# Performance work log

Hardware: AMD Instinct MI355X
Metric: run time of the kernel (lower is better)

The kernel has to match this reference:

```python
import jax, jax.numpy as jnp
import numpy as np

B, N0, D0, N1, D1 = 128, 64, 32, 64, 32
K = 65  # depthwise conv kernel size
SCALE = 5.0
FOCUS = 3.0
EPS_Z = float(jnp.finfo(jnp.float32).eps)


def setup_inputs() -> dict:
    key = jax.random.key(0)
    k1, k2, k3, kw, kc, kb = jax.random.split(key, 6)
    x1 = jax.random.normal(k1, (B, N0, D0), dtype=jnp.float32)
    x2 = jax.random.normal(k2, (B, N0, D0), dtype=jnp.float32)
    x3 = jax.random.normal(k3, (B, N0, D0), dtype=jnp.float32)
    # kaiming_normal_ on W [N1, N0, D0, D1]: fan_in = N0*D0*D1 per torch default on 4D
    fan_in = N0 * D0 * D1
    W = jax.random.normal(kw, (N1, N0, D0, D1), dtype=jnp.float32) * np.sqrt(2.0 / fan_in)
    # Conv1d(N1*D1, N1*D1, K, groups=N1): weight [out_ch, in_ch/groups, K]
    cin_g = D1
    bound = 1.0 / np.sqrt(cin_g * K)
    conv_w = jax.random.uniform(kc, (N1 * D1, cin_g, K), dtype=jnp.float32, minval=-bound, maxval=bound)
    conv_b = jax.random.uniform(kb, (N1 * D1,), dtype=jnp.float32, minval=-bound, maxval=bound)
    return {"x1": x1, "x2": x2, "x3": x3, "W": W, "conv_w": conv_w, "conv_b": conv_b}


def _transform(x, W):
    # x: [B, N0, D0], W: [N1, N0, D0, D1] -> u: [B, N1*D1, N0]
    u = jnp.einsum('bji,kjiz->bkjz', x, W)        # [B, N1, N0, D1]
    u = jnp.transpose(u, (0, 1, 3, 2))             # [B, N1, D1, N0]
    return u.reshape(u.shape[0], N1 * D1, N0)


def _focus(u):
    # ReLU kernel + focusing-factor renormalization along last dim
    u = jax.nn.relu(u) + 1e-6
    u = u / SCALE
    n = jnp.linalg.norm(u, axis=-1, keepdims=True)
    up = u ** FOCUS
    return up / jnp.linalg.norm(up, axis=-1, keepdims=True) * n


def _squash(x, eps=1e-20):
    norm = jnp.linalg.norm(x, axis=-1, keepdims=True)
    coef = 1.0 - 1.0 / (jnp.exp(norm) + eps)
    return coef * (x / (norm + eps))


def reference(x1, x2, x3, W, conv_w, conv_b):
    u1 = _focus(_transform(x1, W))  # [B, N1*D1, N0]
    u2 = _focus(_transform(x2, W))
    u3 = _focus(_transform(x3, W))
    z = 1.0 / (jnp.einsum('bic,bc->bi', u1, u1.sum(axis=1)) + EPS_Z)  # [B, N1*D1]
    kv = jnp.einsum('bjc,bjd->bcd', u2, u3)                           # [B, N0, N0]
    x = jnp.einsum('bic,bcd,bi->bid', u1, kv, z)                      # [B, N1*D1, N0]
    # grouped (depthwise-per-capsule) conv1d, 'same' padding
    y = jax.lax.conv_general_dilated(
        x, conv_w, window_strides=(1,), padding=[(K // 2, K // 2)],
        dimension_numbers=('NCH', 'OIH', 'NCH'), feature_group_count=N1)
    y = y + conv_b[None, :, None]
    out = (x + y).sum(axis=-1).reshape(-1, N1, D1)  # [B, N1, D1]
    return _squash(out)
```

## Files before the change

### kernel.cpp

```cpp
#include <hip/hip_runtime.h>
#include <cstddef>

#define NB 128
#define NT 64
#define ND 32
#define NG 64
#define NC 2048
#define KW 65
#define EPSZ 1.1920928955078125e-07f

#define OFF_URAW 0ull
#define SZ_URAW  (3ull * NB * NT * NC)
#define OFF_F    (OFF_URAW + SZ_URAW)
#define SZ_F     (3ull * NB * NC)
#define OFF_S1   (OFF_F + SZ_F)
#define SZ_S1    ((unsigned long long)NB * NT)
#define OFF_KV   (OFF_S1 + SZ_S1)
#define SZ_KV    ((unsigned long long)NB * NT * NT)

__global__ __launch_bounds__(256) void k_transform(
    const float* __restrict__ x1, const float* __restrict__ x2,
    const float* __restrict__ x3, const float* __restrict__ W,
    float* __restrict__ uraw) {
  int bid = blockIdx.x;
  int j   = bid & 63;
  int nt  = (bid >> 6) & 15;
  int inp = bid >> 10;
  const float* x = (inp == 0) ? x1 : ((inp == 1) ? x2 : x3);
  float* uout = uraw + (size_t)inp * ((size_t)NB * NT * NC);

  __shared__ float as[32][132];
  __shared__ float bs[32][132];
  int tid = threadIdx.x;

  {
    int b = tid >> 1, h = tid & 1;
    const float* xp = x + ((size_t)b * NT + j) * ND + h * 16;
#pragma unroll
    for (int q = 0; q < 4; ++q) {
      float4 v = *reinterpret_cast<const float4*>(xp + q * 4);
      int i0 = h * 16 + q * 4;
      as[i0 + 0][b] = v.x; as[i0 + 1][b] = v.y;
      as[i0 + 2][b] = v.z; as[i0 + 3][b] = v.w;
    }
  }
  {
    int kk = tid >> 6, u = tid & 63;
    int i = u >> 1, h = u & 1;
    const float* wp = W + (((size_t)(nt * 4 + kk) * NT + j) * ND + i) * ND + h * 16;
#pragma unroll
    for (int q = 0; q < 4; ++q) {
      float4 v = *reinterpret_cast<const float4*>(wp + q * 4);
      int c0 = kk * 32 + h * 16 + q * 4;
      bs[i][c0 + 0] = v.x; bs[i][c0 + 1] = v.y;
      bs[i][c0 + 2] = v.z; bs[i][c0 + 3] = v.w;
    }
  }
  __syncthreads();

  int tm = tid & 15, tn = tid >> 4;
  int m0 = tm * 8, n0 = tn * 8;
  float acc[8][8];
#pragma unroll
  for (int a = 0; a < 8; ++a)
#pragma unroll
    for (int c = 0; c < 8; ++c) acc[a][c] = 0.f;

#pragma unroll 4
  for (int kk = 0; kk < 32; ++kk) {
    float4 a0 = *reinterpret_cast<const float4*>(&as[kk][m0]);
    float4 a1 = *reinterpret_cast<const float4*>(&as[kk][m0 + 4]);
    float4 b0 = *reinterpret_cast<const float4*>(&bs[kk][n0]);
    float4 b1 = *reinterpret_cast<const float4*>(&bs[kk][n0 + 4]);
    float av[8] = {a0.x, a0.y, a0.z, a0.w, a1.x, a1.y, a1.z, a1.w};
    float bv[8] = {b0.x, b0.y, b0.z, b0.w, b1.x, b1.y, b1.z, b1.w};
#pragma unroll
    for (int mi = 0; mi < 8; ++mi)
#pragma unroll
      for (int ni = 0; ni < 8; ++ni)
        acc[mi][ni] = fmaf(av[mi], bv[ni], acc[mi][ni]);
  }

#pragma unroll
  for (int mi = 0; mi < 8; ++mi) {
    float* cp = uout + ((size_t)(m0 + mi) * NT + j) * NC + nt * 128 + n0;
    float4 v0 = {acc[mi][0], acc[mi][1], acc[mi][2], acc[mi][3]};
    float4 v1 = {acc[mi][4], acc[mi][5], acc[mi][6], acc[mi][7]};
    *reinterpret_cast<float4*>(cp)     = v0;
    *reinterpret_cast<float4*>(cp + 4) = v1;
  }
}

__global__ __launch_bounds__(256) void k_factors(
    const float* __restrict__ uraw, float* __restrict__ f,
    float* __restrict__ s1) {
  int bid = blockIdx.x;
  int q = bid & 3, b = (bid >> 2) & 127, inp = bid >> 9;
  const float* u = uraw + ((size_t)inp * NB + b) * ((size_t)NT * NC);
  int tid = threadIdx.x;
  int ch = q * 512 + tid * 2;

  float s2a = 0.f, s6a = 0.f, s2b = 0.f, s6b = 0.f;
  for (int t = 0; t < NT; ++t) {
    float2 v = *reinterpret_cast<const float2*>(u + (size_t)t * NC + ch);
    float ua = (fmaxf(v.x, 0.f) + 1e-6f) * 0.2f;
    float p2a = ua * ua, p3a = p2a * ua;
    s2a += p2a; s6a += p3a * p3a;
    float ub = (fmaxf(v.y, 0.f) + 1e-6f) * 0.2f;
    float p2b = ub * ub, p3b = p2b * ub;
    s2b += p2b; s6b += p3b * p3b;
  }
  float fa = sqrtf(s2a) / sqrtf(s6a);
  float fb = sqrtf(s2b) / sqrtf(s6b);
  float2 fv = {fa, fb};
  *reinterpret_cast<float2*>(f + ((size_t)inp * NB + b) * NC + ch) = fv;

  if (inp == 0) {
    __shared__ float part[NT][4];
    int wid = tid >> 6, lane = tid & 63;
    for (int t = 0; t < NT; ++t) {
      float2 v = *reinterpret_cast<const float2*>(u + (size_t)t * NC + ch);
      float ua = (fmaxf(v.x, 0.f) + 1e-6f) * 0.2f;
      float ub = (fmaxf(v.y, 0.f) + 1e-6f) * 0.2f;
      float val = ua * ua * ua * fa + ub * ub * ub * fb;
#pragma unroll
      for (int m = 32; m >= 1; m >>= 1) val += __shfl_xor(val, m, 64);
      if (lane == 0) part[t][wid] = val;
    }
    __syncthreads();
    if (tid < NT)
      atomicAdd(&s1[b * NT + tid],
                part[tid][0] + part[tid][1] + part[tid][2] + part[tid][3]);
  }
}

__global__ void k_zero(float* __restrict__ p, int n) {
  int i = blockIdx.x * blockDim.x + threadIdx.x;
  int stride = gridDim.x * blockDim.x;
  for (; i < n; i += stride) p[i] = 0.f;
}

__global__ __launch_bounds__(256) void k_kv(
    const float* __restrict__ uraw, const float* __restrict__ f,
    float* __restrict__ kv) {
  int b = blockIdx.x >> 3, chq = blockIdx.x & 7;
  int chbase = chq * 256;
  const float* u2 = uraw + ((size_t)NB + b) * ((size_t)NT * NC);
  const float* u3 = uraw + (2ull * NB + b) * ((size_t)NT * NC);
  const float* f2 = f + ((size_t)NB + b) * NC;
  const float* f3 = f + (2ull * NB + b) * NC;

  __shared__ float a2[64][68];
  __shared__ float a3[64][68];
  int tid = threadIdx.x;

  int tm = tid & 15, tn = tid >> 4;
  float acc[4][4];
#pragma unroll
  for (int r = 0; r < 4; ++r)
#pragma unroll
    for (int q = 0; q < 4; ++q) acc[r][q] = 0.f;

  for (int tile = 0; tile < 4; ++tile) {
    int ch0 = chbase + tile * 64;
    __syncthreads();
    {
      int t = tid >> 2, c4 = tid & 3;
#pragma unroll
      for (int q = 0; q < 4; ++q) {
        int c = c4 * 16 + q * 4;
        float4 v2 = *reinterpret_cast<const float4*>(u2 + (size_t)t * NC + ch0 + c);
        float4 g2 = *reinterpret_cast<const float4*>(f2 + ch0 + c);
        float4 v3 = *reinterpret_cast<const float4*>(u3 + (size_t)t * NC + ch0 + c);
        float4 g3 = *reinterpret_cast<const float4*>(f3 + ch0 + c);
        float vv2[4] = {v2.x, v2.y, v2.z, v2.w};
        float gg2[4] = {g2.x, g2.y, g2.z, g2.w};
        float vv3[4] = {v3.x, v3.y, v3.z, v3.w};
        float gg3[4] = {g3.x, g3.y, g3.z, g3.w};
#pragma unroll
        for (int r = 0; r < 4; ++r) {
          float uu = (fmaxf(vv2[r], 0.f) + 1e-6f) * 0.2f;
          a2[c + r][t] = uu * uu * uu * gg2[r];
          float ww = (fmaxf(vv3[r], 0.f) + 1e-6f) * 0.2f;
          a3[c + r][t] = ww * ww * ww * gg3[r];
        }
      }
    }
    __syncthreads();
#pragma unroll 8
    for (int ch = 0; ch < 64; ++ch) {
      float4 av = *reinterpret_cast<const float4*>(&a2[ch][tm * 4]);
      float4 bv = *reinterpret_cast<const float4*>(&a3[ch][tn * 4]);
      float aa[4] = {av.x, av.y, av.z, av.w};
      float bb[4] = {bv.x, bv.y, bv.z, bv.w};
#pragma unroll
      for (int r = 0; r < 4; ++r)
#pragma unroll
        for (int q = 0; q < 4; ++q)
          acc[r][q] = fmaf(aa[r], bb[q], acc[r][q]);
    }
  }
#pragma unroll
  for (int r = 0; r < 4; ++r)
#pragma unroll
    for (int q = 0; q < 4; ++q)
      atomicAdd(&kv[(size_t)b * (NT * NT) + (tm * 4 + r) * NT + tn * 4 + q],
                acc[r][q]);
}

__global__ __launch_bounds__(64) void k_cwt(
    const float* __restrict__ cw, float* __restrict__ cwt) {
  int o = blockIdx.x;
  int tid = threadIdx.x;
  __shared__ float row[32 * KW];
  for (int i = tid; i < 32 * KW; i += 64) row[i] = cw[(size_t)o * (32 * KW) + i];
  __syncthreads();
  int jj = tid, j = jj + 1;
  for (int ci = 0; ci < 32; ++ci) {
    float v = 0.f;
    if (j <= 32) v -= row[ci * KW + j + 32];
    if (j >= 32 && j <= 63) v += row[ci * KW + j - 32];
    if (j == 64) {
      float s = 0.f;
      for (int k = 32; k <= 64; ++k) s += row[ci * KW + k];
      v += s;
    }
    cwt[(size_t)o * 2048 + ci * 64 + jj] = v;
  }
}

__global__ __launch_bounds__(256) void k_pre(
    const float* __restrict__ uraw, const float* __restrict__ f,
    const float* __restrict__ kvg, const float* __restrict__ s1g,
    float* __restrict__ pre) {
  int b = blockIdx.x >> 3, q = blockIdx.x & 7;
  int chbase = q * 256;
  const float* u1 = uraw + (size_t)b * ((size_t)NT * NC);
  const float* f1 = f + (size_t)b * NC;
  int tid = threadIdx.x;

  __shared__ float kvpreL[64][68];
  __shared__ float s1L[64];
  __shared__ float utL[64][132];

#pragma unroll
  for (int qq = 0; qq < 16; ++qq) {
    int i = tid + qq * 256;
    kvpreL[i >> 6][i & 63] = kvg[(size_t)b * (NT * NT) + i];
  }
  if (tid < 64) s1L[tid] = s1g[b * NT + tid];
  __syncthreads();
  if (tid < 64) {
    float run = 0.f;
    for (int t2 = 0; t2 < 64; ++t2) {
      run += kvpreL[tid][t2];
      kvpreL[tid][t2] = run;
    }
  }

  int cg = tid >> 3, tg = tid & 7;
  for (int tile = 0; tile < 2; ++tile) {
    int ch0 = chbase + tile * 128;
    __syncthreads();
    {
      int t = tid >> 2, c4 = tid & 3;
      const float* up = u1 + (size_t)t * NC + ch0 + c4 * 32;
      const float* fp = f1 + ch0 + c4 * 32;
#pragma unroll
      for (int qq = 0; qq < 8; ++qq) {
        float4 v  = *reinterpret_cast<const float4*>(up + qq * 4);
        float4 fv = *reinterpret_cast<const float4*>(fp + qq * 4);
        float vv[4] = {v.x, v.y, v.z, v.w};
        float ff[4] = {fv.x, fv.y, fv.z, fv.w};
#pragma unroll
        for (int r = 0; r < 4; ++r) {
          float uu = (fmaxf(vv[r], 0.f) + 1e-6f) * 0.2f;
          utL[t][c4 * 33 + qq * 4 + r] = uu * uu * uu * ff[r];
        }
      }
    }
    __syncthreads();

    int cl = cg * 4;
    int sk = (cl >> 5) * 33 + (cl & 31);
    float acc[4][8];
#pragma unroll
    for (int r = 0; r < 4; ++r)
#pragma unroll
      for (int c = 0; c < 8; ++c) acc[r][c] = 0.f;
    float accz[4] = {0.f, 0.f, 0.f, 0.f};

#pragma unroll 4
    for (int t1 = 0; t1 < 64; ++t1) {
      float4 a = *reinterpret_cast<const float4*>(&utL[t1][sk]);
      float s = s1L[t1];
      float4 k0 = *reinterpret_cast<const float4*>(&kvpreL[t1][tg * 8]);
      float4 k1 = *reinterpret_cast<const float4*>(&kvpreL[t1][tg * 8 + 4]);
      float aa[4] = {a.x, a.y, a.z, a.w};
      float kk[8] = {k0.x, k0.y, k0.z, k0.w, k1.x, k1.y, k1.z, k1.w};
#pragma unroll
      for (int r = 0; r < 4; ++r) {
        accz[r] = fmaf(aa[r], s, accz[r]);
#pragma unroll
        for (int c = 0; c < 8; ++c)
          acc[r][c] = fmaf(aa[r], kk[c], acc[r][c]);
      }
    }
#pragma unroll
    for (int r = 0; r < 4; ++r) {
      float z = 1.f / (accz[r] + EPSZ);
      float* pp = pre + ((size_t)b * NC + ch0 + cl + r) * 64 + tg * 8;
      float4 o0 = {acc[r][0] * z, acc[r][1] * z, acc[r][2] * z, acc[r][3] * z};
      float4 o1 = {acc[r][4] * z, acc[r][5] * z, acc[r][6] * z, acc[r][7] * z};
      *reinterpret_cast<float4*>(pp)     = o0;
      *reinterpret_cast<float4*>(pp + 4) = o1;
    }
  }
}

__global__ __launch_bounds__(256) void k_gemm(
    const float* __restrict__ pre, const float* __restrict__ cwt,
    float* __restrict__ ysum) {
  int g = blockIdx.x >> 3, ks = blockIdx.x & 7;
  int tid = threadIdx.x;
  int oh = tid & 7, bh = tid >> 3;

  __shared__ float AsT[64][132];
  __shared__ float BsT[64][36];

  float acc[4][4];
#pragma unroll
  for (int i = 0; i < 4; ++i)
#pragma unroll
    for (int j = 0; j < 4; ++j) acc[i][j] = 0.f;

  for (int kc = 0; kc < 4; ++kc) {
    int ci = ks * 4 + kc;
    __syncthreads();
    {
      int bb = tid >> 1, jh = (tid & 1) * 32;
      const float* ap = pre + ((size_t)bb * NC + g * 32 + ci) * 64 + jh;
#pragma unroll
      for (int qq = 0; qq < 8; ++qq) {
        float4 v = *reinterpret_cast<const float4*>(ap + qq * 4);
        int jj = jh + qq * 4;
        AsT[jj + 0][bb] = v.x; AsT[jj + 1][bb] = v.y;
        AsT[jj + 2][bb] = v.z; AsT[jj + 3][bb] = v.w;
      }
    }
    if (tid < 128) {
      int o = tid >> 2, jh = (tid & 3) * 16;
      const float* bp = cwt + (size_t)(g * 32 + o) * 2048 + ci * 64 + jh;
#pragma unroll
      for (int qq = 0; qq < 4; ++qq) {
        float4 v = *reinterpret_cast<const float4*>(bp + qq * 4);
        int jj = jh + qq * 4;
        BsT[jj + 0][o] = v.x; BsT[jj + 1][o] = v.y;
        BsT[jj + 2][o] = v.z; BsT[jj + 3][o] = v.w;
      }
    }
    __syncthreads();

#pragma unroll 8
    for (int jj = 0; jj < 64; ++jj) {
      float4 a = *reinterpret_cast<const float4*>(&AsT[jj][bh * 4]);
      float4 bv = *reinterpret_cast<const float4*>(&BsT[jj][oh * 4]);
      float aa[4] = {a.x, a.y, a.z, a.w};
      float bb[4] = {bv.x, bv.y, bv.z, bv.w};
#pragma unroll
      for (int i = 0; i < 4; ++i)
#pragma unroll
        for (int j = 0; j < 4; ++j)
          acc[i][j] = fmaf(aa[i], bb[j], acc[i][j]);
    }
  }

#pragma unroll
  for (int i = 0; i < 4; ++i)
#pragma unroll
    for (int j = 0; j < 4; ++j)
      atomicAdd(&ysum[(size_t)(bh * 4 + i) * NC + g * 32 + oh * 4 + j],
                acc[i][j]);
}

__global__ __launch_bounds__(256) void k_out(
    const float* __restrict__ pre, const float* __restrict__ ysum,
    const float* __restrict__ cb, float* __restrict__ out) {
  int tid = threadIdx.x;
  int b = blockIdx.x >> 3;
  int g = (blockIdx.x & 7) * 8 + (tid >> 5);
  int o = tid & 31;
  int go = g * 32 + o;
  float xs = pre[((size_t)b * NC + go) * 64 + 63];
  float val = ysum[(size_t)b * NC + go] + xs + 64.f * cb[go];
  float sq = val * val;
#pragma unroll
  for (int m = 16; m >= 1; m >>= 1) sq += __shfl_xor(sq, m, 32);
  float norm = sqrtf(sq);
  float coef = 1.f - 1.f / (expf(norm) + 1e-20f);
  out[((size_t)b * NG + g) * ND + o] = coef * val / (norm + 1e-20f);
}

extern "C" void kernel_launch(void* const* d_in, const int* in_sizes, int n_in,
                              void* d_out, int out_size, void* d_ws, size_t ws_size,
                              hipStream_t stream) {
  const float* x1 = (const float*)d_in[0];
  const float* x2 = (const float*)d_in[1];
  const float* x3 = (const float*)d_in[2];
  const float* W  = (const float*)d_in[3];
  const float* cw = (const float*)d_in[4];
  const float* cb = (const float*)d_in[5];
  float* out = (float*)d_out;

  float* ws   = (float*)d_ws;
  float* uraw = ws + OFF_URAW;
  float* f    = ws + OFF_F;
  float* s1   = ws + OFF_S1;
  float* kv   = ws + OFF_KV;
  float* pre  = uraw + (size_t)NB * NT * NC;
  float* cwt  = uraw + 2ull * NB * NT * NC;
  float* ysum = uraw;

  k_transform<<<3072, 256, 0, stream>>>(x1, x2, x3, W, uraw);
  k_zero<<<256, 256, 0, stream>>>(s1, (int)(SZ_S1 + SZ_KV));
  k_factors<<<1536, 256, 0, stream>>>(uraw, f, s1);
  k_kv<<<1024, 256, 0, stream>>>(uraw, f, kv);
  k_cwt<<<2048, 64, 0, stream>>>(cw, cwt);
  k_pre<<<1024, 256, 0, stream>>>(uraw, f, kv, s1, pre);
  k_zero<<<256, 256, 0, stream>>>(ysum, (int)(NB * NC));
  k_gemm<<<512, 256, 0, stream>>>(pre, cwt, ysum);
  k_out<<<1024, 256, 0, stream>>>(pre, ysum, cb, out);
}
```

Before: 397.4 us.

## Restructure kv kernel to per-wave 8x8 register tiles with split-K waves

The kv Gram kernel now gives each wave its own 64-channel slice, staged in private shared buffers, with every lane computing an 8x8 output tile instead of a block-wide 4x4 tiling. The four waves' partial results are reduced pairwise in shared memory before atomics go to global memory, so each block issues half as many atomics. The aim is more register-level reuse per shared-memory load and less global atomic traffic. In exchange it needs 64 accumulators per thread, which raises register pressure, and it adds extra barriers.

New measurement: 596.7 us. 50.1% more time.

```diff
diff --git a/kernel.cpp b/kernel.cpp
--- a/kernel.cpp
+++ b/kernel.cpp
@@ -17,6 +17,11 @@
 #define SZ_S1    ((unsigned long long)NB * NT)
 #define OFF_KV   (OFF_S1 + SZ_S1)
 #define SZ_KV    ((unsigned long long)NB * NT * NT)
+
+__device__ __forceinline__ float foc(float v, float fv) {
+  float u = (fmaxf(v, 0.f) + 1e-6f) * 0.2f;
+  return u * u * u * fv;
+}
 
 __global__ __launch_bounds__(256) void k_transform(
     const float* __restrict__ x1, const float* __restrict__ x2,
@@ -143,69 +148,84 @@
 __global__ __launch_bounds__(256) void k_kv(
     const float* __restrict__ uraw, const float* __restrict__ f,
     float* __restrict__ kv) {
-  int b = blockIdx.x >> 3, chq = blockIdx.x & 7;
-  int chbase = chq * 256;
+  int b = blockIdx.x >> 3, ks = blockIdx.x & 7;
+  int wv = threadIdx.x >> 6, lane = threadIdx.x & 63;
   const float* u2 = uraw + ((size_t)NB + b) * ((size_t)NT * NC);
   const float* u3 = uraw + (2ull * NB + b) * ((size_t)NT * NC);
   const float* f2 = f + ((size_t)NB + b) * NC;
   const float* f3 = f + (2ull * NB + b) * NC;
 
-  __shared__ float a2[64][68];
-  __shared__ float a3[64][68];
-  int tid = threadIdx.x;
-
-  int tm = tid & 15, tn = tid >> 4;
-  float acc[4][4];
-#pragma unroll
-  for (int r = 0; r < 4; ++r)
-#pragma unroll
-    for (int q = 0; q < 4; ++q) acc[r][q] = 0.f;
-
-  for (int tile = 0; tile < 4; ++tile) {
-    int ch0 = chbase + tile * 64;
-    __syncthreads();
-    {
-      int t = tid >> 2, c4 = tid & 3;
-#pragma unroll
-      for (int q = 0; q < 4; ++q) {
-        int c = c4 * 16 + q * 4;
-        float4 v2 = *reinterpret_cast<const float4*>(u2 + (size_t)t * NC + ch0 + c);
-        float4 g2 = *reinterpret_cast<const float4*>(f2 + ch0 + c);
-        float4 v3 = *reinterpret_cast<const float4*>(u3 + (size_t)t * NC + ch0 + c);
-        float4 g3 = *reinterpret_cast<const float4*>(f3 + ch0 + c);
-        float vv2[4] = {v2.x, v2.y, v2.z, v2.w};
-        float gg2[4] = {g2.x, g2.y, g2.z, g2.w};
-        float vv3[4] = {v3.x, v3.y, v3.z, v3.w};
-        float gg3[4] = {g3.x, g3.y, g3.z, g3.w};
-#pragma unroll
-        for (int r = 0; r < 4; ++r) {
-          float uu = (fmaxf(vv2[r], 0.f) + 1e-6f) * 0.2f;
-          a2[c + r][t] = uu * uu * uu * gg2[r];
-          float ww = (fmaxf(vv3[r], 0.f) + 1e-6f) * 0.2f;
-          a3[c + r][t] = ww * ww * ww * gg3[r];
-        }
-      }
-    }
-    __syncthreads();
-#pragma unroll 8
-    for (int ch = 0; ch < 64; ++ch) {
-      float4 av = *reinterpret_cast<const float4*>(&a2[ch][tm * 4]);
-      float4 bv = *reinterpret_cast<const float4*>(&a3[ch][tn * 4]);
-      float aa[4] = {av.x, av.y, av.z, av.w};
-      float bb[4] = {bv.x, bv.y, bv.z, bv.w};
-#pragma unroll
-      for (int r = 0; r < 4; ++r)
-#pragma unroll
-        for (int q = 0; q < 4; ++q)
-          acc[r][q] = fmaf(aa[r], bb[q], acc[r][q]);
-    }
-  }
-#pragma unroll
-  for (int r = 0; r < 4; ++r)
-#pragma unroll
-    for (int q = 0; q < 4; ++q)
-      atomicAdd(&kv[(size_t)b * (NT * NT) + (tm * 4 + r) * NT + tn * 4 + q],
-                acc[r][q]);
+  __shared__ float sbuf[4][2][64][18];
+
+  int tm = lane >> 3, tn = lane & 7;
+  int tq = lane >> 2, q = lane & 3;
+
+  float acc[8][8];
+#pragma unroll
+  for (int i = 0; i < 8; ++i)
+#pragma unroll
+    for (int j = 0; j < 8; ++j) acc[i][j] = 0.f;
+
+  for (int chunk = 0; chunk < 4; ++chunk) {
+    int ch0 = ks * 256 + wv * 64 + chunk * 16;
+    float4 f2q = *reinterpret_cast<const float4*>(f2 + ch0 + q * 4);
+    float4 f3q = *reinterpret_cast<const float4*>(f3 + ch0 + q * 4);
+    __syncthreads();
+#pragma unroll
+    for (int p = 0; p < 4; ++p) {
+      int t = p * 16 + tq;
+      float4 v2 = *reinterpret_cast<const float4*>(u2 + (size_t)t * NC + ch0 + q * 4);
+      float4 v3 = *reinterpret_cast<const float4*>(u3 + (size_t)t * NC + ch0 + q * 4);
+      float* w2 = &sbuf[wv][0][t][q * 4];
+      float* w3 = &sbuf[wv][1][t][q * 4];
+      float2 a0 = {foc(v2.x, f2q.x), foc(v2.y, f2q.y)};
+      float2 a1 = {foc(v2.z, f2q.z), foc(v2.w, f2q.w)};
+      float2 c0 = {foc(v3.x, f3q.x), foc(v3.y, f3q.y)};
+      float2 c1 = {foc(v3.z, f3q.z), foc(v3.w, f3q.w)};
+      *reinterpret_cast<float2*>(w2)     = a0;
+      *reinterpret_cast<float2*>(w2 + 2) = a1;
+      *reinterpret_cast<float2*>(w3)     = c0;
+      *reinterpret_cast<float2*>(w3 + 2) = c1;
+    }
+    __syncthreads();
+
+#pragma unroll
+    for (int k = 0; k < 8; ++k) {
+      float2 af[8], bf[8];
+#pragma unroll
+      for (int i = 0; i < 8; ++i)
+        af[i] = *reinterpret_cast<const float2*>(&sbuf[wv][0][tm * 8 + i][k * 2]);
+#pragma unroll
+      for (int j = 0; j < 8; ++j)
+        bf[j] = *reinterpret_cast<const float2*>(&sbuf[wv][1][tn * 8 + j][k * 2]);
+#pragma unroll
+      for (int i = 0; i < 8; ++i)
+#pragma unroll
+        for (int j = 0; j < 8; ++j)
+          acc[i][j] = fmaf(af[i].y, bf[j].y, fmaf(af[i].x, bf[j].x, acc[i][j]));
+    }
+  }
+
+  float* xch = &sbuf[0][0][0][0];
+  float* tile = xch + (wv >> 1) * (64 * 66);
+  __syncthreads();
+  if ((wv & 1) == 0) {
+#pragma unroll
+    for (int i = 0; i < 8; ++i)
+#pragma unroll
+      for (int j = 0; j < 8; ++j)
+        tile[(tm * 8 + i) * 66 + tn * 8 + j] = acc[i][j];
+  }
+  __syncthreads();
+  if (wv & 1) {
+    float* kvp = kv + (size_t)b * (NT * NT);
+#pragma unroll
+    for (int i = 0; i < 8; ++i)
+#pragma unroll
+      for (int j = 0; j < 8; ++j)
+        atomicAdd(&kvp[(tm * 8 + i) * 64 + tn * 8 + j],
+                  acc[i][j] + tile[(tm * 8 + i) * 66 + tn * 8 + j]);
+  }
 }
 
 __global__ __launch_bounds__(64) void k_cwt(
```
